# Optimization experiments

Hardware: AMD Instinct MI355X
Metric: run time of the kernel (lower is better)

The kernel has to match this reference:

```python
import jax, jax.numpy as jnp
import numpy as np

N_EMBD = 768
N_HEAD = 8
HEAD_DIM = N_EMBD // N_HEAD
EPS = 1e-5


def _layernorm(x, g, b):
    mu = jnp.mean(x, axis=-1, keepdims=True)
    var = jnp.mean(jnp.square(x - mu), axis=-1, keepdims=True)
    return (x - mu) * jax.lax.rsqrt(var + EPS) * g + b


def _new_gelu(x):
    c = jnp.sqrt(2.0 / jnp.pi).astype(x.dtype)
    return 0.5 * x * (1.0 + jnp.tanh(c * (x + 0.044715 * x * x * x)))


def setup_inputs() -> dict:
    key = jax.random.key(0)
    ks = jax.random.split(key, 10)
    B, T, C = 16, 1024, N_EMBD
    s = lambda fan_in: 1.0 / np.sqrt(fan_in)
    inp = {
        "x": jax.random.normal(ks[0], (B, T, C), dtype=jnp.float32),
        "ln1_g": jnp.ones((C,), jnp.float32),
        "ln1_b": jnp.zeros((C,), jnp.float32),
        "attn_w": jax.random.normal(ks[1], (C, 3 * C), jnp.float32) * s(C),
        "attn_b": jnp.zeros((3 * C,), jnp.float32),
        "proj_w": jax.random.normal(ks[2], (C, C), jnp.float32) * s(C),
        "proj_b": jnp.zeros((C,), jnp.float32),
        "ln2_g": jnp.ones((C,), jnp.float32),
        "ln2_b": jnp.zeros((C,), jnp.float32),
        "fc_w": jax.random.normal(ks[3], (C, 4 * C), jnp.float32) * s(C),
        "fc_b": jnp.zeros((4 * C,), jnp.float32),
        "fc2_w": jax.random.normal(ks[4], (4 * C, C), jnp.float32) * s(4 * C),
        "fc2_b": jnp.zeros((C,), jnp.float32),
    }
    return inp


def reference(x, ln1_g, ln1_b, attn_w, attn_b, proj_w, proj_b,
              ln2_g, ln2_b, fc_w, fc_b, fc2_w, fc2_b):
    B, T, C = x.shape
    H, D = N_HEAD, HEAD_DIM
    scale = 1.0 / np.sqrt(D)

    # --- attention branch ---
    h = _layernorm(x, ln1_g, ln1_b)
    qkv = h @ attn_w + attn_b                       # [B,T,3C]
    q, k, v = jnp.split(qkv, 3, axis=-1)
    q = q.reshape(B, T, H, D).transpose(0, 2, 1, 3)  # [B,H,T,D]
    k = k.reshape(B, T, H, D).transpose(0, 2, 1, 3)
    v = v.reshape(B, T, H, D).transpose(0, 2, 1, 3)
    att = jnp.einsum("bhqd,bhkd->bhqk", q, k) * scale
    causal = jnp.tril(jnp.ones((T, T), bool))
    att = jnp.where(causal, att, -jnp.inf)
    att = jax.nn.softmax(att, axis=-1)
    y = jnp.einsum("bhqk,bhkd->bhqd", att, v)        # [B,H,T,D]
    y = y.transpose(0, 2, 1, 3).reshape(B, T, C)
    y = y @ proj_w + proj_b
    x = x + y

    # --- MLP branch ---
    h2 = _layernorm(x, ln2_g, ln2_b)
    h2 = _new_gelu(h2 @ fc_w + fc_b)
    x = x + (h2 @ fc2_w + fc2_b)
    return x
```

## Files before the change

### kernel.cpp

```cpp
#include <hip/hip_runtime.h>


typedef __bf16 bf16;
typedef __bf16 bf16x8 __attribute__((ext_vector_type(8)));
typedef __bf16 bf16x4 __attribute__((ext_vector_type(4)));
typedef __bf16 bf16x2 __attribute__((ext_vector_type(2)));
typedef float f32x4 __attribute__((ext_vector_type(4)));

__device__ __forceinline__ void async_copy16(const void* g, void* l)
{
    __builtin_amdgcn_global_load_lds((__attribute__((address_space(1))) void*)g,
                                     (__attribute__((address_space(3))) void*)l,
                                     16, 0, 0);
}

__global__ __launch_bounds__(256) void wtrans(const float* __restrict__ in,
                                              bf16* __restrict__ out,
                                              const int R, const int C)
{
    __shared__ float tile[32][33];
    const int c0 = blockIdx.x * 32, r0 = blockIdx.y * 32;
    const int tx = threadIdx.x, ty = threadIdx.y;
#pragma unroll
    for (int i = 0; i < 4; ++i)
        tile[ty + i * 8][tx] = in[(size_t)(r0 + ty + i * 8) * C + c0 + tx];
    __syncthreads();
#pragma unroll
    for (int i = 0; i < 4; ++i)
        out[(size_t)(c0 + ty + i * 8) * R + r0 + tx] = (bf16)tile[tx][ty + i * 8];
}

template <typename TIN>
__global__ __launch_bounds__(256) void ln_kernel(const TIN* __restrict__ x,
                                                 const float* __restrict__ g,
                                                 const float* __restrict__ bb,
                                                 bf16* __restrict__ out)
{
    const int wave = threadIdx.x >> 6, lane = threadIdx.x & 63;
    const size_t row = (size_t)blockIdx.x * 4 + wave;
    const TIN* xr = x + row * 768;
    float v[12];
    float s = 0.f;
#pragma unroll
    for (int c = 0; c < 3; ++c) {
        if constexpr (sizeof(TIN) == 2) {
            const bf16x4 t4 = *(const bf16x4*)(xr + c * 256 + lane * 4);
#pragma unroll
            for (int j = 0; j < 4; ++j) { v[c * 4 + j] = (float)t4[j]; s += v[c * 4 + j]; }
        } else {
            const float4 t4 = *(const float4*)(xr + c * 256 + lane * 4);
            v[c * 4 + 0] = t4.x; v[c * 4 + 1] = t4.y;
            v[c * 4 + 2] = t4.z; v[c * 4 + 3] = t4.w;
            s += t4.x + t4.y + t4.z + t4.w;
        }
    }
#pragma unroll
    for (int off = 32; off >= 1; off >>= 1) s += __shfl_xor(s, off, 64);
    const float mu = s * (1.f / 768.f);
    float q = 0.f;
#pragma unroll
    for (int i = 0; i < 12; ++i) { const float d = v[i] - mu; q += d * d; }
#pragma unroll
    for (int off = 32; off >= 1; off >>= 1) q += __shfl_xor(q, off, 64);
    const float rs = rsqrtf(q * (1.f / 768.f) + 1e-5f);
#pragma unroll
    for (int c = 0; c < 3; ++c) {
        const float4 gv = *(const float4*)(g + c * 256 + lane * 4);
        const float4 bv = *(const float4*)(bb + c * 256 + lane * 4);
        bf16x4 ov;
        ov[0] = (bf16)((v[c * 4 + 0] - mu) * rs * gv.x + bv.x);
        ov[1] = (bf16)((v[c * 4 + 1] - mu) * rs * gv.y + bv.y);
        ov[2] = (bf16)((v[c * 4 + 2] - mu) * rs * gv.z + bv.z);
        ov[3] = (bf16)((v[c * 4 + 3] - mu) * rs * gv.w + bv.w);
        *(bf16x4*)(out + row * 768 + c * 256 + lane * 4) = ov;
    }
}

template <int EPI, int TN>
__global__ __launch_bounds__(256) void gemm_bt(const bf16* __restrict__ A,
                                               const bf16* __restrict__ Bt,
                                               const float* __restrict__ bias,
                                               const void* __restrict__ res,
                                               void* __restrict__ out,
                                               const int M, const int N, const int K)
{
    constexpr int NT_W = TN / 32;
    constexpr int NCPB = (TN * 8) / 256;
    __shared__ bf16 sA[2 * 128 * 32];
    __shared__ bf16 sB[2 * TN * 32];
    const int t = threadIdx.x;
    const int wave = t >> 6, lane = t & 63;
    const int quad = lane >> 4, l16 = lane & 15;
    const int bm0 = blockIdx.y * 128, bn0 = blockIdx.x * TN;
    const int wm = (wave >> 1) * 64, wn = (wave & 1) * (TN / 2);

    const f32x4 z4 = {0.f, 0.f, 0.f, 0.f};
    f32x4 acc[4][NT_W];
#pragma unroll
    for (int i = 0; i < 4; ++i)
#pragma unroll
        for (int j = 0; j < NT_W; ++j) acc[i][j] = z4;

    const bf16* gAp[4]; bf16* lAp[4];
#pragma unroll
    for (int c = 0; c < 4; ++c) {
        const int j = c * 256 + t;
        const int img = j >> 9, r = (j >> 2) & 127, k8 = j & 3;
        gAp[c] = A + (size_t)(bm0 + r) * K + img * 32 + k8 * 8;
        lAp[c] = sA + j * 8;
    }
    const bf16* gBp[NCPB]; bf16* lBp[NCPB];
#pragma unroll
    for (int c = 0; c < NCPB; ++c) {
        const int j = c * 256 + t;
        const int img = j / (TN * 4), r = (j % (TN * 4)) >> 2, k8 = j & 3;
        gBp[c] = Bt + (size_t)(bn0 + r) * K + img * 32 + k8 * 8;
        lBp[c] = sB + j * 8;
    }

    for (int kt = 0; kt < K; kt += 64) {
        __syncthreads();
#pragma unroll
        for (int c = 0; c < 4; ++c) async_copy16(gAp[c] + kt, lAp[c]);
#pragma unroll
        for (int c = 0; c < NCPB; ++c) async_copy16(gBp[c] + kt, lBp[c]);
        __syncthreads();

#pragma unroll
        for (int ks = 0; ks < 2; ++ks) {
            bf16x8 af[4], bfm[NT_W];
#pragma unroll
            for (int mt = 0; mt < 4; ++mt)
                af[mt] = *(const bf16x8*)(sA + ks * 4096 +
                                          (wm + mt * 16 + l16) * 32 + quad * 8);
#pragma unroll
            for (int nt = 0; nt < NT_W; ++nt)
                bfm[nt] = *(const bf16x8*)(sB + ks * (TN * 32) +
                                           (wn + nt * 16 + l16) * 32 + quad * 8);
#pragma unroll
            for (int mt = 0; mt < 4; ++mt)
#pragma unroll
                for (int nt = 0; nt < NT_W; ++nt)
                    acc[mt][nt] = __builtin_amdgcn_mfma_f32_16x16x32_bf16(
                        af[mt], bfm[nt], acc[mt][nt], 0, 0, 0);
        }
    }

    const int rb = bm0 + wm + quad * 4;
    const int cb = bn0 + wn + l16;
#pragma unroll
    for (int mt = 0; mt < 4; ++mt) {
#pragma unroll
        for (int nt = 0; nt < NT_W; ++nt) {
            const int col = cb + nt * 16;
            const float bv = bias[col];
#pragma unroll
            for (int reg = 0; reg < 4; ++reg) {
                const size_t idx = (size_t)(rb + mt * 16 + reg) * N + col;
                float v = acc[mt][nt][reg] + bv;
                if constexpr (EPI == 1) {
                    ((bf16*)out)[idx] = (bf16)(v + ((const float*)res)[idx]);
                } else if constexpr (EPI == 2) {
                    const float u = v;
                    const float a2 = 1.5957691216057308f *
                                     (u + 0.044715f * u * u * u);
                    v = u / (1.f + __expf(-a2));
                    ((bf16*)out)[idx] = (bf16)v;
                } else if constexpr (EPI == 3) {
                    ((float*)out)[idx] = v + (float)((const bf16*)res)[idx];
                } else {
                    ((bf16*)out)[idx] = (bf16)v;
                }
            }
        }
    }
}

__global__ __launch_bounds__(256) void attn_kernel(const bf16* __restrict__ qkv,
                                                   bf16* __restrict__ aout)
{
    constexpr int T = 1024, C3 = 2304, HD = 96, CC = 768;
    __shared__ bf16 sK[64 * 104];
    __shared__ bf16 sV[96 * 72];
    __shared__ bf16 sP[4][16 * 76];
    const int tid = threadIdx.x;
    const int wave = tid >> 6, lane = tid & 63;
    const int quad = lane >> 4, l16 = lane & 15;
    const int bh = blockIdx.y, b = bh >> 3, h = bh & 7;
    const float scale = 0.10206207261596575f;

    const int qAi = blockIdx.x;
    const int qBi = 15 - qAi;
    const int q0A = qAi * 64 + wave * 16;
    const int q0B = qBi * 64 + wave * 16;

    const bf16* kgbase = qkv + (size_t)b * T * C3 + CC + h * HD;
    const bf16* vgbase = qkv + (size_t)b * T * C3 + 2 * CC + h * HD;
    bf16* sPw = &sP[wave][0];

    int kKey[3], kCh[3], vKey2[3], vDq[3];
#pragma unroll
    for (int c = 0; c < 3; ++c) {
        const int j = c * 256 + tid;
        kKey[c] = j / 12; kCh[c] = j - kKey[c] * 12;
        vKey2[c] = (j & 31) * 2; vDq[c] = j >> 5;
    }

    const bf16* qrA = qkv + (size_t)(b * T + q0A + l16) * C3 + h * HD + quad * 8;
    const bf16* qrB = qkv + (size_t)(b * T + q0B + l16) * C3 + h * HD + quad * 8;
    const bf16x8 aQA0 = *(const bf16x8*)(qrA);
    const bf16x8 aQA1 = *(const bf16x8*)(qrA + 32);
    const bf16x8 aQA2 = *(const bf16x8*)(qrA + 64);
    const bf16x8 aQB0 = *(const bf16x8*)(qrB);
    const bf16x8 aQB1 = *(const bf16x8*)(qrB + 32);
    const bf16x8 aQB2 = *(const bf16x8*)(qrB + 64);

    const f32x4 z4 = {0.f, 0.f, 0.f, 0.f};
    f32x4 oA[6], oB[6];
#pragma unroll
    for (int i = 0; i < 6; ++i) { oA[i] = z4; oB[i] = z4; }
    float lA[4] = {0.f, 0.f, 0.f, 0.f}, lB[4] = {0.f, 0.f, 0.f, 0.f};

    auto process = [&](const bf16x8& Q0, const bf16x8& Q1, const bf16x8& Q2,
                       f32x4 (&o)[6], float (&lrow)[4],
                       const int q0, const int kk0) {
        f32x4 s[4];
#pragma unroll
        for (int i = 0; i < 4; ++i) s[i] = z4;
#pragma unroll
        for (int nt = 0; nt < 4; ++nt) {
            const bf16* kp = sK + (nt * 16 + l16) * 104 + quad * 8;
            const bf16x8 b0 = *(const bf16x8*)(kp);
            const bf16x8 b1 = *(const bf16x8*)(kp + 32);
            const bf16x8 b2 = *(const bf16x8*)(kp + 64);
            s[nt] = __builtin_amdgcn_mfma_f32_16x16x32_bf16(Q0, b0, s[nt], 0, 0, 0);
            s[nt] = __builtin_amdgcn_mfma_f32_16x16x32_bf16(Q1, b1, s[nt], 0, 0, 0);
            s[nt] = __builtin_amdgcn_mfma_f32_16x16x32_bf16(Q2, b2, s[nt], 0, 0, 0);
        }

        float psum[4] = {0.f, 0.f, 0.f, 0.f};
#pragma unroll
        for (int nt = 0; nt < 4; ++nt)
#pragma unroll
            for (int reg = 0; reg < 4; ++reg) {
                const int qr = q0 + quad * 4 + reg;
                const int key = kk0 + nt * 16 + l16;
                float v = s[nt][reg] * scale;
                v = (key > qr) ? -1e30f : v;
                const float p = __expf(fminf(v, 30.f));
                s[nt][reg] = p;
                psum[reg] += p;
            }

#pragma unroll
        for (int nt = 0; nt < 4; ++nt)
#pragma unroll
            for (int reg = 0; reg < 4; ++reg)
                sPw[(quad * 4 + reg) * 76 + nt * 16 + l16] = (bf16)s[nt][reg];
        __asm__ volatile("s_waitcnt lgkmcnt(0)" ::: "memory");

#pragma unroll
        for (int off = 1; off < 16; off <<= 1)
#pragma unroll
            for (int reg = 0; reg < 4; ++reg)
                psum[reg] += __shfl_xor(psum[reg], off, 64);
#pragma unroll
        for (int reg = 0; reg < 4; ++reg) lrow[reg] += psum[reg];

        const bf16x8 aP0 = *(const bf16x8*)(sPw + l16 * 76 + quad * 8);
        const bf16x8 aP1 = *(const bf16x8*)(sPw + l16 * 76 + 32 + quad * 8);
#pragma unroll
        for (int dd = 0; dd < 6; ++dd) {
            const bf16* vp = sV + (dd * 16 + l16) * 72 + quad * 8;
            const bf16x8 v0 = *(const bf16x8*)(vp);
            const bf16x8 v1 = *(const bf16x8*)(vp + 32);
            o[dd] = __builtin_amdgcn_mfma_f32_16x16x32_bf16(aP0, v0, o[dd], 0, 0, 0);
            o[dd] = __builtin_amdgcn_mfma_f32_16x16x32_bf16(aP1, v1, o[dd], 0, 0, 0);
        }
    };

    for (int kb = 0; kb <= qBi; ++kb) {
        const int kk0 = kb * 64;

        __syncthreads();
#pragma unroll
        for (int c = 0; c < 3; ++c) {
            const bf16x8 kv = *(const bf16x8*)(kgbase +
                                (size_t)(kk0 + kKey[c]) * C3 + kCh[c] * 8);
            *(bf16x8*)(sK + kKey[c] * 104 + kCh[c] * 8) = kv;
        }
#pragma unroll
        for (int c = 0; c < 3; ++c) {
            const bf16* p0 = vgbase + (size_t)(kk0 + vKey2[c]) * C3 + vDq[c] * 4;
            const bf16x4 va = *(const bf16x4*)p0;
            const bf16x4 vb = *(const bf16x4*)(p0 + C3);
#pragma unroll
            for (int jj = 0; jj < 4; ++jj) {
                bf16x2 pk; pk[0] = va[jj]; pk[1] = vb[jj];
                *(bf16x2*)(sV + (vDq[c] * 4 + jj) * 72 + vKey2[c]) = pk;
            }
        }
        __syncthreads();

        process(aQB0, aQB1, aQB2, oB, lB, q0B, kk0);
        if (kb <= qAi)
            process(aQA0, aQA1, aQA2, oA, lA, q0A, kk0);
    }

    bf16* opA = aout + (size_t)(b * T + q0A + quad * 4) * CC + h * HD + l16;
    bf16* opB = aout + (size_t)(b * T + q0B + quad * 4) * CC + h * HD + l16;
#pragma unroll
    for (int reg = 0; reg < 4; ++reg) {
        const float invA = 1.f / lA[reg];
        const float invB = 1.f / lB[reg];
#pragma unroll
        for (int dd = 0; dd < 6; ++dd) {
            opA[(size_t)reg * CC + dd * 16] = (bf16)(oA[dd][reg] * invA);
            opB[(size_t)reg * CC + dd * 16] = (bf16)(oB[dd][reg] * invB);
        }
    }
}

extern "C" void kernel_launch(void* const* d_in, const int* in_sizes, int n_in,
                              void* d_out, int out_size, void* d_ws, size_t ws_size,
                              hipStream_t stream)
{
    const float* x      = (const float*)d_in[0];
    const float* ln1_g  = (const float*)d_in[1];
    const float* ln1_b  = (const float*)d_in[2];
    const float* attn_w = (const float*)d_in[3];
    const float* attn_b = (const float*)d_in[4];
    const float* proj_w = (const float*)d_in[5];
    const float* proj_b = (const float*)d_in[6];
    const float* ln2_g  = (const float*)d_in[7];
    const float* ln2_b  = (const float*)d_in[8];
    const float* fc_w   = (const float*)d_in[9];
    const float* fc_b   = (const float*)d_in[10];
    const float* fc2_w  = (const float*)d_in[11];
    const float* fc2_b  = (const float*)d_in[12];

    char* ws = (char*)d_ws;
    bf16*  attn_wT = (bf16*)(ws + 0);
    bf16*  proj_wT = (bf16*)(ws + 3538944);
    bf16*  fc_wT   = (bf16*)(ws + 4718592);
    bf16*  fc2_wT  = (bf16*)(ws + 9437184);
    bf16*  hbuf    = (bf16*)(ws + 14155776);
    bf16*  qkv     = (bf16*)(ws + 39321600);
    bf16*  x1      = (bf16*)(ws + 39321600);
    bf16*  act     = (bf16*)(ws + 64487424);

    const dim3 tb(32, 8);

    wtrans<<<dim3(72, 24), tb, 0, stream>>>(attn_w, attn_wT, 768, 2304);
    wtrans<<<dim3(24, 24), tb, 0, stream>>>(proj_w, proj_wT, 768, 768);
    wtrans<<<dim3(96, 24), tb, 0, stream>>>(fc_w, fc_wT, 768, 3072);
    wtrans<<<dim3(24, 96), tb, 0, stream>>>(fc2_w, fc2_wT, 3072, 768);

    ln_kernel<float><<<4096, 256, 0, stream>>>(x, ln1_g, ln1_b, hbuf);

    gemm_bt<0, 128><<<dim3(18, 128), 256, 0, stream>>>(
        hbuf, attn_wT, attn_b, nullptr, qkv, 16384, 2304, 768);

    attn_kernel<<<dim3(8, 128), 256, 0, stream>>>(qkv, hbuf);

    gemm_bt<1, 128><<<dim3(6, 128), 256, 0, stream>>>(
        hbuf, proj_wT, proj_b, x, x1, 16384, 768, 768);

    ln_kernel<bf16><<<4096, 256, 0, stream>>>(x1, ln2_g, ln2_b, hbuf);

    for (int c = 0; c < 2; ++c) {
        const size_t ro = (size_t)c * 8192;
        gemm_bt<2, 128><<<dim3(24, 64), 256, 0, stream>>>(
            hbuf + ro * 768, fc_wT, fc_b, nullptr, act, 8192, 3072, 768);
        gemm_bt<3, 64><<<dim3(12, 64), 256, 0, stream>>>(
            act, fc2_wT, fc2_b, x1 + ro * 768,
            (float*)d_out + ro * 768, 8192, 768, 3072);
    }
}
```

Baseline: 674.2 us.

## Split paired q-tiles into one tile per block and prefetch next K/V tile

The attention kernel stops pairing q-tile i with q-tile 15-i in one block. It now launches 16 blocks per head, each handling one q-tile. The next K/V tile is loaded into registers while the current one is computed, so global-load latency overlaps with the MFMA work. The causal mask is now applied only on the diagonal tile. This doubles block count and drops the load balancing the pairing gave, which may leave uneven work per block, and each block holds more registers for the prefetch.

After: 723.1 us. 1.07x slower.

```diff
diff --git a/kernel.cpp b/kernel.cpp
--- a/kernel.cpp
+++ b/kernel.cpp
@@ -189,10 +189,8 @@
     const int bh = blockIdx.y, b = bh >> 3, h = bh & 7;
     const float scale = 0.10206207261596575f;
 
-    const int qAi = blockIdx.x;
-    const int qBi = 15 - qAi;
-    const int q0A = qAi * 64 + wave * 16;
-    const int q0B = qBi * 64 + wave * 16;
+    const int qi = blockIdx.x;
+    const int q0 = qi * 64 + wave * 16;
 
     const bf16* kgbase = qkv + (size_t)b * T * C3 + CC + h * HD;
     const bf16* vgbase = qkv + (size_t)b * T * C3 + 2 * CC + h * HD;
@@ -206,24 +204,53 @@
         vKey2[c] = (j & 31) * 2; vDq[c] = j >> 5;
     }
 
-    const bf16* qrA = qkv + (size_t)(b * T + q0A + l16) * C3 + h * HD + quad * 8;
-    const bf16* qrB = qkv + (size_t)(b * T + q0B + l16) * C3 + h * HD + quad * 8;
-    const bf16x8 aQA0 = *(const bf16x8*)(qrA);
-    const bf16x8 aQA1 = *(const bf16x8*)(qrA + 32);
-    const bf16x8 aQA2 = *(const bf16x8*)(qrA + 64);
-    const bf16x8 aQB0 = *(const bf16x8*)(qrB);
-    const bf16x8 aQB1 = *(const bf16x8*)(qrB + 32);
-    const bf16x8 aQB2 = *(const bf16x8*)(qrB + 64);
+    const bf16* qr = qkv + (size_t)(b * T + q0 + l16) * C3 + h * HD + quad * 8;
+    const bf16x8 aQ0 = *(const bf16x8*)(qr);
+    const bf16x8 aQ1 = *(const bf16x8*)(qr + 32);
+    const bf16x8 aQ2 = *(const bf16x8*)(qr + 64);
 
     const f32x4 z4 = {0.f, 0.f, 0.f, 0.f};
-    f32x4 oA[6], oB[6];
-#pragma unroll
-    for (int i = 0; i < 6; ++i) { oA[i] = z4; oB[i] = z4; }
-    float lA[4] = {0.f, 0.f, 0.f, 0.f}, lB[4] = {0.f, 0.f, 0.f, 0.f};
-
-    auto process = [&](const bf16x8& Q0, const bf16x8& Q1, const bf16x8& Q2,
-                       f32x4 (&o)[6], float (&lrow)[4],
-                       const int q0, const int kk0) {
+    f32x4 o[6];
+#pragma unroll
+    for (int i = 0; i < 6; ++i) o[i] = z4;
+    float lrow[4] = {0.f, 0.f, 0.f, 0.f};
+
+    bf16x8 kreg[3];
+    bf16x4 va[3], vb[3];
+
+    auto issue_tile = [&](const int kk0) {
+#pragma unroll
+        for (int c = 0; c < 3; ++c) {
+            kreg[c] = *(const bf16x8*)(kgbase + (size_t)(kk0 + kKey[c]) * C3 +
+                                       kCh[c] * 8);
+            const bf16* p0 = vgbase + (size_t)(kk0 + vKey2[c]) * C3 + vDq[c] * 4;
+            va[c] = *(const bf16x4*)p0;
+            vb[c] = *(const bf16x4*)(p0 + C3);
+        }
+    };
+
+    issue_tile(0);
+
+    for (int kb = 0; kb <= qi; ++kb) {
+        const int kk0 = kb * 64;
+        __syncthreads();
+
+#pragma unroll
+        for (int c = 0; c < 3; ++c)
+            *(bf16x8*)(sK + kKey[c] * 104 + kCh[c] * 8) = kreg[c];
+#pragma unroll
+        for (int c = 0; c < 3; ++c) {
+#pragma unroll
+            for (int jj = 0; jj < 4; ++jj) {
+                bf16x2 pk; pk[0] = va[c][jj]; pk[1] = vb[c][jj];
+                *(bf16x2*)(sV + (vDq[c] * 4 + jj) * 72 + vKey2[c]) = pk;
+            }
+        }
+
+        if (kb < qi) issue_tile(kk0 + 64);
+
+        __syncthreads();
+
         f32x4 s[4];
 #pragma unroll
         for (int i = 0; i < 4; ++i) s[i] = z4;
@@ -233,20 +260,23 @@
             const bf16x8 b0 = *(const bf16x8*)(kp);
             const bf16x8 b1 = *(const bf16x8*)(kp + 32);
             const bf16x8 b2 = *(const bf16x8*)(kp + 64);
-            s[nt] = __builtin_amdgcn_mfma_f32_16x16x32_bf16(Q0, b0, s[nt], 0, 0, 0);
-            s[nt] = __builtin_amdgcn_mfma_f32_16x16x32_bf16(Q1, b1, s[nt], 0, 0, 0);
-            s[nt] = __builtin_amdgcn_mfma_f32_16x16x32_bf16(Q2, b2, s[nt], 0, 0, 0);
-        }
-
+            s[nt] = __builtin_amdgcn_mfma_f32_16x16x32_bf16(aQ0, b0, s[nt], 0, 0, 0);
+            s[nt] = __builtin_amdgcn_mfma_f32_16x16x32_bf16(aQ1, b1, s[nt], 0, 0, 0);
+            s[nt] = __builtin_amdgcn_mfma_f32_16x16x32_bf16(aQ2, b2, s[nt], 0, 0, 0);
+        }
+
+        const bool diag = (kb == qi);
         float psum[4] = {0.f, 0.f, 0.f, 0.f};
 #pragma unroll
         for (int nt = 0; nt < 4; ++nt)
 #pragma unroll
             for (int reg = 0; reg < 4; ++reg) {
-                const int qr = q0 + quad * 4 + reg;
-                const int key = kk0 + nt * 16 + l16;
                 float v = s[nt][reg] * scale;
-                v = (key > qr) ? -1e30f : v;
+                if (diag) {
+                    const int qrow = q0 + quad * 4 + reg;
+                    const int key = kk0 + nt * 16 + l16;
+                    v = (key > qrow) ? -1e30f : v;
+                }
                 const float p = __expf(fminf(v, 30.f));
                 s[nt][reg] = p;
                 psum[reg] += p;
@@ -277,47 +307,15 @@
             o[dd] = __builtin_amdgcn_mfma_f32_16x16x32_bf16(aP0, v0, o[dd], 0, 0, 0);
             o[dd] = __builtin_amdgcn_mfma_f32_16x16x32_bf16(aP1, v1, o[dd], 0, 0, 0);
         }
-    };
-
-    for (int kb = 0; kb <= qBi; ++kb) {
-        const int kk0 = kb * 64;
-
-        __syncthreads();
-#pragma unroll
-        for (int c = 0; c < 3; ++c) {
-            const bf16x8 kv = *(const bf16x8*)(kgbase +
-                                (size_t)(kk0 + kKey[c]) * C3 + kCh[c] * 8);
-            *(bf16x8*)(sK + kKey[c] * 104 + kCh[c] * 8) = kv;
-        }
-#pragma unroll
-        for (int c = 0; c < 3; ++c) {
-            const bf16* p0 = vgbase + (size_t)(kk0 + vKey2[c]) * C3 + vDq[c] * 4;
-            const bf16x4 va = *(const bf16x4*)p0;
-            const bf16x4 vb = *(const bf16x4*)(p0 + C3);
-#pragma unroll
-            for (int jj = 0; jj < 4; ++jj) {
-                bf16x2 pk; pk[0] = va[jj]; pk[1] = vb[jj];
-                *(bf16x2*)(sV + (vDq[c] * 4 + jj) * 72 + vKey2[c]) = pk;
-            }
-        }
-        __syncthreads();
-
-        process(aQB0, aQB1, aQB2, oB, lB, q0B, kk0);
-        if (kb <= qAi)
-            process(aQA0, aQA1, aQA2, oA, lA, q0A, kk0);
-    }
-
-    bf16* opA = aout + (size_t)(b * T + q0A + quad * 4) * CC + h * HD + l16;
-    bf16* opB = aout + (size_t)(b * T + q0B + quad * 4) * CC + h * HD + l16;
+    }
+
+    bf16* op = aout + (size_t)(b * T + q0 + quad * 4) * CC + h * HD + l16;
 #pragma unroll
     for (int reg = 0; reg < 4; ++reg) {
-        const float invA = 1.f / lA[reg];
-        const float invB = 1.f / lB[reg];
-#pragma unroll
-        for (int dd = 0; dd < 6; ++dd) {
-            opA[(size_t)reg * CC + dd * 16] = (bf16)(oA[dd][reg] * invA);
-            opB[(size_t)reg * CC + dd * 16] = (bf16)(oB[dd][reg] * invB);
-        }
+        const float inv = 1.f / lrow[reg];
+#pragma unroll
+        for (int dd = 0; dd < 6; ++dd)
+            op[(size_t)reg * CC + dd * 16] = (bf16)(o[dd][reg] * inv);
     }
 }
 
@@ -361,7 +359,7 @@
     gemm_bt<0, 128><<<dim3(18, 128), 256, 0, stream>>>(
         hbuf, attn_wT, attn_b, nullptr, qkv, 16384, 2304, 768);
 
-    attn_kernel<<<dim3(8, 128), 256, 0, stream>>>(qkv, hbuf);
+    attn_kernel<<<dim3(16, 128), 256, 0, stream>>>(qkv, hbuf);
 
     gemm_bt<1, 128><<<dim3(6, 128), 256, 0, stream>>>(
         hbuf, proj_wT, proj_b, x, x1, 16384, 768, 768);
```

## Prefetch next K/V tile into registers in attention, skip masks off-diagonal

Applied to the files above, without the earlier changes.

The attention kernel now issues global loads for the next K/V tile into registers before computing on the current one. This overlaps memory latency with MFMA work, and barriers are changed to not drain outstanding vector loads. The causal mask is applied only on diagonal blocks. The grid is transposed so that blocks for the same query pair across heads are scheduled together, and launch bounds request 4 blocks per CU. In exchange the kernel holds more registers for the prefetched tile, and correctness depends on the custom barrier and waitcnt ordering.

Result: slower. 766.4 us (+13.7%).

```diff
diff --git a/kernel.cpp b/kernel.cpp
--- a/kernel.cpp
+++ b/kernel.cpp
@@ -12,6 +12,15 @@
     __builtin_amdgcn_global_load_lds((__attribute__((address_space(1))) void*)g,
                                      (__attribute__((address_space(3))) void*)l,
                                      16, 0, 0);
+}
+
+__device__ __forceinline__ void bar_nodrain()
+{
+    __builtin_amdgcn_sched_barrier(0);
+    __asm__ volatile("" ::: "memory");
+    __builtin_amdgcn_s_barrier();
+    __asm__ volatile("" ::: "memory");
+    __builtin_amdgcn_sched_barrier(0);
 }
 
 __global__ __launch_bounds__(256) void wtrans(const float* __restrict__ in,
@@ -176,8 +185,8 @@
     }
 }
 
-__global__ __launch_bounds__(256) void attn_kernel(const bf16* __restrict__ qkv,
-                                                   bf16* __restrict__ aout)
+__global__ __launch_bounds__(256, 4) void attn_kernel(const bf16* __restrict__ qkv,
+                                                      bf16* __restrict__ aout)
 {
     constexpr int T = 1024, C3 = 2304, HD = 96, CC = 768;
     __shared__ bf16 sK[64 * 104];
@@ -186,10 +195,10 @@
     const int tid = threadIdx.x;
     const int wave = tid >> 6, lane = tid & 63;
     const int quad = lane >> 4, l16 = lane & 15;
-    const int bh = blockIdx.y, b = bh >> 3, h = bh & 7;
+    const int bh = blockIdx.x, b = bh >> 3, h = bh & 7;
     const float scale = 0.10206207261596575f;
 
-    const int qAi = blockIdx.x;
+    const int qAi = blockIdx.y;
     const int qBi = 15 - qAi;
     const int q0A = qAi * 64 + wave * 16;
     const int q0B = qBi * 64 + wave * 16;
@@ -221,9 +230,22 @@
     for (int i = 0; i < 6; ++i) { oA[i] = z4; oB[i] = z4; }
     float lA[4] = {0.f, 0.f, 0.f, 0.f}, lB[4] = {0.f, 0.f, 0.f, 0.f};
 
+    bf16x8 kreg[3];
+    bf16x4 va[3], vb[3];
+    auto issue_tile = [&](const int kk0) {
+#pragma unroll
+        for (int c = 0; c < 3; ++c) {
+            kreg[c] = *(const bf16x8*)(kgbase + (size_t)(kk0 + kKey[c]) * C3 +
+                                       kCh[c] * 8);
+            const bf16* p0 = vgbase + (size_t)(kk0 + vKey2[c]) * C3 + vDq[c] * 4;
+            va[c] = *(const bf16x4*)p0;
+            vb[c] = *(const bf16x4*)(p0 + C3);
+        }
+    };
+
     auto process = [&](const bf16x8& Q0, const bf16x8& Q1, const bf16x8& Q2,
                        f32x4 (&o)[6], float (&lrow)[4],
-                       const int q0, const int kk0) {
+                       const int q0, const int kk0, const bool diag) {
         f32x4 s[4];
 #pragma unroll
         for (int i = 0; i < 4; ++i) s[i] = z4;
@@ -243,10 +265,12 @@
         for (int nt = 0; nt < 4; ++nt)
 #pragma unroll
             for (int reg = 0; reg < 4; ++reg) {
-                const int qr = q0 + quad * 4 + reg;
-                const int key = kk0 + nt * 16 + l16;
                 float v = s[nt][reg] * scale;
-                v = (key > qr) ? -1e30f : v;
+                if (diag) {
+                    const int qr = q0 + quad * 4 + reg;
+                    const int key = kk0 + nt * 16 + l16;
+                    v = (key > qr) ? -1e30f : v;
+                }
                 const float p = __expf(fminf(v, 30.f));
                 s[nt][reg] = p;
                 psum[reg] += p;
@@ -279,32 +303,33 @@
         }
     };
 
+    issue_tile(0);
+
     for (int kb = 0; kb <= qBi; ++kb) {
         const int kk0 = kb * 64;
 
-        __syncthreads();
+        bar_nodrain();
+
+#pragma unroll
+        for (int c = 0; c < 3; ++c)
+            *(bf16x8*)(sK + kKey[c] * 104 + kCh[c] * 8) = kreg[c];
 #pragma unroll
         for (int c = 0; c < 3; ++c) {
-            const bf16x8 kv = *(const bf16x8*)(kgbase +
-                                (size_t)(kk0 + kKey[c]) * C3 + kCh[c] * 8);
-            *(bf16x8*)(sK + kKey[c] * 104 + kCh[c] * 8) = kv;
-        }
-#pragma unroll
-        for (int c = 0; c < 3; ++c) {
-            const bf16* p0 = vgbase + (size_t)(kk0 + vKey2[c]) * C3 + vDq[c] * 4;
-            const bf16x4 va = *(const bf16x4*)p0;
-            const bf16x4 vb = *(const bf16x4*)(p0 + C3);
 #pragma unroll
             for (int jj = 0; jj < 4; ++jj) {
-                bf16x2 pk; pk[0] = va[jj]; pk[1] = vb[jj];
+                bf16x2 pk; pk[0] = va[c][jj]; pk[1] = vb[c][jj];
                 *(bf16x2*)(sV + (vDq[c] * 4 + jj) * 72 + vKey2[c]) = pk;
             }
         }
-        __syncthreads();
-
-        process(aQB0, aQB1, aQB2, oB, lB, q0B, kk0);
+
+        if (kb < qBi) issue_tile(kk0 + 64);
+
+        __asm__ volatile("s_waitcnt lgkmcnt(0)" ::: "memory");
+        bar_nodrain();
+
+        process(aQB0, aQB1, aQB2, oB, lB, q0B, kk0, kb == qBi);
         if (kb <= qAi)
-            process(aQA0, aQA1, aQA2, oA, lA, q0A, kk0);
+            process(aQA0, aQA1, aQA2, oA, lA, q0A, kk0, kb == qAi);
     }
 
     bf16* opA = aout + (size_t)(b * T + q0A + quad * 4) * CC + h * HD + l16;
@@ -361,7 +386,7 @@
     gemm_bt<0, 128><<<dim3(18, 128), 256, 0, stream>>>(
         hbuf, attn_wT, attn_b, nullptr, qkv, 16384, 2304, 768);
 
-    attn_kernel<<<dim3(8, 128), 256, 0, stream>>>(qkv, hbuf);
+    attn_kernel<<<dim3(128, 8), 256, 0, stream>>>(qkv, hbuf);
 
     gemm_bt<1, 128><<<dim3(6, 128), 256, 0, stream>>>(
         hbuf, proj_wT, proj_b, x, x1, 16384, 768, 768);
```
